# Optimization experiments

Hardware: AMD Instinct MI355X
Metric: run time of the kernel (lower is better)

The kernel has to match this reference:

```python
import jax, jax.numpy as jnp
import numpy as np

TOP_K = 2

def _moe_forward(x, gate_w, w1, w2, w3):
    # x: [B,S,H] -> tokens [T,H]
    B, S, H = x.shape
    xt = x.reshape(-1, H)                              # [T,H]
    T = xt.shape[0]
    E = gate_w.shape[0]
    # router
    logits = xt @ gate_w.T                             # [T,E]
    probs = jax.nn.softmax(logits.astype(jnp.float32), axis=-1)
    rw, sel = jax.lax.top_k(probs, TOP_K)              # [T,K]
    rw = rw / jnp.sum(rw, axis=-1, keepdims=True)
    # per-token per-expert combine weight (0 if expert not selected)
    combine = jnp.zeros((T, E), dtype=xt.dtype).at[
        jnp.arange(T)[:, None], sel].add(rw.astype(xt.dtype))  # [T,E]
    # dense per-expert SwiGLU FFN over all tokens (prefill path of module)
    h1 = jnp.einsum('th,efh->tef', xt, w1)             # [T,E,F]
    h3 = jnp.einsum('th,efh->tef', xt, w3)             # [T,E,F]
    g = jax.nn.silu(h1) * h3                           # [T,E,F]
    g = g * combine[:, :, None]                        # apply routing weight before down-proj
    out = jnp.einsum('tef,ehf->th', g, w2)             # [T,H]
    return out.reshape(B, S, H)


def setup_inputs() -> dict:
    key = jax.random.key(0)
    ks = jax.random.split(key, 5)
    B, S, H, F, E = 2, 2048, 1024, 3584, 8
    scale = 1.0 / np.sqrt(H)
    return {
        'hidden_states': jax.random.normal(ks[0], (B, S, H), jnp.float32),
        'gate_w': jax.random.normal(ks[1], (E, H), jnp.float32) * scale,
        'w1': jax.random.normal(ks[2], (E, F, H), jnp.float32) * scale,
        'w2': jax.random.normal(ks[3], (E, H, F), jnp.float32) * (1.0 / np.sqrt(F)),
        'w3': jax.random.normal(ks[4], (E, F, H), jnp.float32) * scale,
    }


def reference(hidden_states, gate_w, w1, w2, w3):
    return _moe_forward(hidden_states, gate_w, w1, w2, w3)
```

## Files before the change

### kernel.cpp

```cpp
#include <hip/hip_runtime.h>
#include <hip/hip_bf16.h>

#define TT   4096
#define HH   1024
#define FF   3584
#define EE   8
#define N13  7168
#define TKP  8192

typedef unsigned short u16;
typedef __attribute__((ext_vector_type(8))) short short8;
typedef __attribute__((ext_vector_type(4))) float floatx4;

__device__ __forceinline__ u16 f2b(float f) {
  union { float f; unsigned u; } v; v.f = f;
  unsigned r = v.u + 0x7FFFu + ((v.u >> 16) & 1u);
  return (u16)(r >> 16);
}

__device__ __forceinline__ void gld_lds16(const u16* g, u16* l) {
  __builtin_amdgcn_global_load_lds((const __attribute__((address_space(1))) unsigned int*)g,
                                   (__attribute__((address_space(3))) unsigned int*)l,
                                   16, 0, 0);
}

#define WAIT_LGKM0() asm volatile("s_waitcnt lgkmcnt(0)" ::: "memory")
#define WAIT_VM(n)   asm volatile("s_waitcnt vmcnt(" #n ")" ::: "memory")
#define BARRIER()    do { asm volatile("" ::: "memory"); __builtin_amdgcn_s_barrier(); asm volatile("" ::: "memory"); } while (0)

__global__ __launch_bounds__(256) void cvt_w13(const float* __restrict__ w1, const float* __restrict__ w3,
                                               ushort4* __restrict__ w13i) {
  int i = blockIdx.x * 256 + threadIdx.x;
  const int perE = N13 * (HH / 4);
  int e = i / perE;
  int rem = i - e * perE;
  int n = rem / (HH / 4);
  int h4 = rem - n * (HH / 4);
  int f = ((n >> 5) << 4) + (n & 15);
  int sel = (n >> 4) & 1;
  const float* base = sel ? w3 : w1;
  const float4* src = ((const float4*)(base + (size_t)(e * FF + f) * HH)) + h4;
  float4 v = *src;
  ushort4 o; o.x = f2b(v.x); o.y = f2b(v.y); o.z = f2b(v.z); o.w = f2b(v.w);
  w13i[i] = o;
}

__global__ __launch_bounds__(256) void cvt_w2(const float4* __restrict__ in, ushort4* __restrict__ outp) {
  int i = blockIdx.x * 256 + threadIdx.x;
  float4 v = in[i];
  ushort4 o; o.x = f2b(v.x); o.y = f2b(v.y); o.z = f2b(v.z); o.w = f2b(v.w);
  outp[i] = o;
}

__global__ __launch_bounds__(256) void router(const float* __restrict__ x, const float* __restrict__ gw,
                                              int* __restrict__ cnt, int* __restrict__ tok_list,
                                              float* __restrict__ wt_list, u16* __restrict__ xb) {
  int lane = threadIdx.x & 63;
  int wv = threadIdx.x >> 6;
  int t = blockIdx.x * 4 + wv;
  const float* xp = x + (size_t)t * HH;
  u16* xbp = xb + (size_t)t * HH;
  float acc[EE];
#pragma unroll
  for (int e = 0; e < EE; e++) acc[e] = 0.f;
  for (int h = lane; h < HH; h += 64) {
    float xv = xp[h];
    xbp[h] = f2b(xv);
#pragma unroll
    for (int e = 0; e < EE; e++) acc[e] += xv * gw[e * HH + h];
  }
#pragma unroll
  for (int e = 0; e < EE; e++) {
#pragma unroll
    for (int off = 32; off > 0; off >>= 1) acc[e] += __shfl_xor(acc[e], off, 64);
  }
  if (lane == 0) {
    int i1 = 0;
#pragma unroll
    for (int e = 1; e < EE; e++) if (acc[e] > acc[i1]) i1 = e;
    int i2 = -1;
#pragma unroll
    for (int e = 0; e < EE; e++) {
      if (e == i1) continue;
      if (i2 < 0 || acc[e] > acc[i2]) i2 = e;
    }
    float wA = 1.f / (1.f + __expf(acc[i2] - acc[i1]));
    float wB = 1.f - wA;
    int p1 = atomicAdd(cnt + i1, 1);
    tok_list[i1 * TT + p1] = t; wt_list[i1 * TT + p1] = wA;
    int p2 = atomicAdd(cnt + i2, 1);
    tok_list[i2 * TT + p2] = t; wt_list[i2 * TT + p2] = wB;
  }
}

__global__ void mk_offsets(const int* __restrict__ cnt, int* __restrict__ offs) {
  if (threadIdx.x == 0) {
    int s = 0;
    for (int e = 0; e < EE; e++) { offs[e] = s; s += cnt[e]; }
  }
}

__global__ __launch_bounds__(256) void pairmap(const int* __restrict__ cnt, const int* __restrict__ offs,
                                               const int* __restrict__ tok_list,
                                               int* __restrict__ tokp) {
  int i = blockIdx.x * 256 + threadIdx.x;
  int e = i >> 12;
  int s = i & (TT - 1);
  if (s < cnt[e]) {
    tokp[offs[e] + s] = tok_list[i];
  }
}

__global__ __launch_bounds__(512, 2) void gemm_a(const u16* __restrict__ xb, const u16* __restrict__ w13i,
                                                 const int* __restrict__ cnt, const int* __restrict__ offs,
                                                 const int* __restrict__ tok_list, const float* __restrict__ wt_list,
                                                 u16* __restrict__ gbuf) {
  const int fid = blockIdx.y * 28 + blockIdx.x;
  const int swz = (fid & 7) * 448 + (fid >> 3);
  const int ntile = swz % 28;
  const int yy = swz / 28;
  const int e = yy >> 4;
  const int rt = yy & 15;
  const int cn = cnt[e];
  if (rt * 256 >= cn) return;

  extern __shared__ char dynsmem[];
  u16* As = (u16*)dynsmem;
  u16* Bs = (u16*)(dynsmem + 65536);
  int* toks = (int*)(dynsmem + 131072);
  float* wts = (float*)(dynsmem + 131072 + 1024);

  const int tid = threadIdx.x;
  if (tid < 256) {
    int r = rt * 256 + tid;
    if (r >= cn) r = cn - 1;
    toks[tid] = tok_list[e * TT + r];
    wts[tid] = wt_list[e * TT + r];
  }
  __syncthreads();

  const int l = (tid & 7) ^ ((tid >> 3) & 7);
  const int dst0 = tid * 8;
  const u16* aS[4];
  const u16* bS[4];
#pragma unroll
  for (int i = 0; i < 4; i++) {
    int row = (tid >> 3) + i * 64;
    aS[i] = xb + (size_t)toks[row] * HH + l * 8;
    bS[i] = w13i + ((size_t)e * N13 + (size_t)ntile * 256 + row) * HH + l * 8;
  }

  auto STAGE = [&](int kt) {
    int b = (kt & 1) * 16384;
#pragma unroll
    for (int i = 0; i < 4; i++) {
      gld_lds16(aS[i] + kt * 64, As + b + dst0 + i * 4096);
      gld_lds16(bS[i] + kt * 64, Bs + b + dst0 + i * 4096);
    }
  };

  const int lane = tid & 63;
  const int wv = tid >> 6;
  const int wr = (wv >> 2) * 128;
  const int wc = (wv & 3) * 64;
  const int fr = lane & 15;
  const int fk8 = lane >> 4;

  floatx4 acc[8][4];
#pragma unroll
  for (int mi = 0; mi < 8; mi++)
#pragma unroll
    for (int ni = 0; ni < 4; ni++)
#pragma unroll
      for (int q = 0; q < 4; q++) acc[mi][ni][q] = 0.f;

  STAGE(0);
  STAGE(1);
  WAIT_VM(8);
  BARRIER();

  for (int t = 0; t < 16; t++) {
    const u16* Ab = As + (t & 1) * 16384;
    const u16* Bb = Bs + (t & 1) * 16384;
    __builtin_amdgcn_s_setprio(1);
#pragma unroll
    for (int ks = 0; ks < 2; ks++) {
      const int co = ((ks * 4 + fk8) ^ (fr & 7)) * 8;
      short8 af[8];
#pragma unroll
      for (int mi = 0; mi < 8; mi++)
        af[mi] = *(const short8*)&Ab[(wr + mi * 16 + fr) * 64 + co];
#pragma unroll
      for (int ni = 0; ni < 4; ni++) {
        short8 bf = *(const short8*)&Bb[(wc + ni * 16 + fr) * 64 + co];
#pragma unroll
        for (int mi = 0; mi < 8; mi++)
          acc[mi][ni] = __builtin_amdgcn_mfma_f32_16x16x32_bf16(af[mi], bf, acc[mi][ni], 0, 0, 0);
      }
    }
    __builtin_amdgcn_s_setprio(0);
    WAIT_LGKM0();
    BARRIER();
    if (t + 2 < 16) {
      STAGE(t + 2);
      WAIT_VM(8);
    } else {
      WAIT_VM(0);
    }
    BARRIER();
  }

  const int gofs = offs[e];
  const int cl = lane & 15;
  const int qr = (lane >> 4) * 4;
#pragma unroll
  for (int mi = 0; mi < 8; mi++) {
#pragma unroll
    for (int q = 0; q < 4; q++) {
      int r = wr + mi * 16 + qr + q;
      int gr = rt * 256 + r;
      if (gr < cn) {
        float w = wts[r];
        u16* dst = gbuf + (size_t)(gofs + gr) * FF + (size_t)ntile * 128 + (wc >> 1) + cl;
#pragma unroll
        for (int pg = 0; pg < 2; pg++) {
          float h1 = acc[mi][2 * pg][q];
          float h3 = acc[mi][2 * pg + 1][q];
          float s = h1 / (1.f + __expf(-h1));
          dst[pg * 16] = f2b(s * h3 * w);
        }
      }
    }
  }
}

__global__ __launch_bounds__(512, 2) void gemm_b(const u16* __restrict__ g, const u16* __restrict__ w2b,
                                                 const int* __restrict__ cnt, const int* __restrict__ offs,
                                                 const int* __restrict__ tokp, float* __restrict__ out) {
  const int fid = blockIdx.y * 8 + blockIdx.x;
  const int swz = (fid & 7) * 128 + (fid >> 3);
  const int ntile = swz % 8;
  const int yy = swz / 8;
  const int e = yy >> 4;
  const int rt = yy & 15;
  const int cn = cnt[e];
  if (rt * 256 >= cn) return;
  const int gofs = offs[e];

  extern __shared__ char dynsmem[];
  u16* As = (u16*)dynsmem;
  u16* Bs = (u16*)(dynsmem + 65536);
  int* toks = (int*)(dynsmem + 65536 + 32768);

  const int tid = threadIdx.x;
  if (tid < 256) {
    int r = rt * 256 + tid;
    if (r >= cn) r = cn - 1;
    toks[tid] = tokp[gofs + r];
  }
  __syncthreads();

  const int l = (tid & 7) ^ ((tid >> 3) & 7);
  const int dst0 = tid * 8;
  const u16* aS[4];
  const u16* bS[2];
#pragma unroll
  for (int i = 0; i < 4; i++) {
    int row = (tid >> 3) + i * 64;
    int gr = rt * 256 + row;
    if (gr >= cn) gr = cn - 1;
    aS[i] = g + (size_t)(gofs + gr) * FF + l * 8;
  }
#pragma unroll
  for (int i = 0; i < 2; i++) {
    int row = (tid >> 3) + i * 64;
    bS[i] = w2b + ((size_t)e * HH + (size_t)ntile * 128 + row) * FF + l * 8;
  }

  auto STAGE = [&](int kt) {
    int ba = (kt & 1) * 16384;
    int bb = (kt & 1) * 8192;
#pragma unroll
    for (int i = 0; i < 4; i++) gld_lds16(aS[i] + kt * 64, As + ba + dst0 + i * 4096);
#pragma unroll
    for (int i = 0; i < 2; i++) gld_lds16(bS[i] + kt * 64, Bs + bb + dst0 + i * 4096);
  };

  const int lane = tid & 63;
  const int wv = tid >> 6;
  const int wr = (wv >> 1) * 64;
  const int wc = (wv & 1) * 64;
  const int fr = lane & 15;
  const int fk8 = lane >> 4;

  floatx4 acc[4][4];
#pragma unroll
  for (int mi = 0; mi < 4; mi++)
#pragma unroll
    for (int ni = 0; ni < 4; ni++)
#pragma unroll
      for (int q = 0; q < 4; q++) acc[mi][ni][q] = 0.f;

  STAGE(0);
  STAGE(1);
  WAIT_VM(6);
  BARRIER();

  for (int t = 0; t < 56; t++) {
    const u16* Ab = As + (t & 1) * 16384;
    const u16* Bb = Bs + (t & 1) * 8192;
    __builtin_amdgcn_s_setprio(1);
#pragma unroll
    for (int ks = 0; ks < 2; ks++) {
      const int co = ((ks * 4 + fk8) ^ (fr & 7)) * 8;
      short8 af[4];
#pragma unroll
      for (int mi = 0; mi < 4; mi++)
        af[mi] = *(const short8*)&Ab[(wr + mi * 16 + fr) * 64 + co];
#pragma unroll
      for (int ni = 0; ni < 4; ni++) {
        short8 bf = *(const short8*)&Bb[(wc + ni * 16 + fr) * 64 + co];
#pragma unroll
        for (int mi = 0; mi < 4; mi++)
          acc[mi][ni] = __builtin_amdgcn_mfma_f32_16x16x32_bf16(af[mi], bf, acc[mi][ni], 0, 0, 0);
      }
    }
    __builtin_amdgcn_s_setprio(0);
    WAIT_LGKM0();
    BARRIER();
    if (t + 2 < 56) {
      STAGE(t + 2);
      WAIT_VM(6);
    } else {
      WAIT_VM(0);
    }
    BARRIER();
  }

  const int cl = lane & 15;
  const int qr = (lane >> 4) * 4;
#pragma unroll
  for (int mi = 0; mi < 4; mi++) {
#pragma unroll
    for (int q = 0; q < 4; q++) {
      int r = wr + mi * 16 + qr + q;
      int gr = rt * 256 + r;
      if (gr < cn) {
        int tk = toks[r];
        float* dst = out + (size_t)tk * HH + (size_t)ntile * 128 + wc + cl;
#pragma unroll
        for (int ni = 0; ni < 4; ni++) atomicAdd(dst + ni * 16, acc[mi][ni][q]);
      }
    }
  }
}

extern "C" void kernel_launch(void* const* d_in, const int* in_sizes, int n_in,
                              void* d_out, int out_size, void* d_ws, size_t ws_size,
                              hipStream_t stream) {
  const float* x  = (const float*)d_in[0];
  const float* gw = (const float*)d_in[1];
  const float* w1 = (const float*)d_in[2];
  const float* w2 = (const float*)d_in[3];
  const float* w3 = (const float*)d_in[4];
  float* out = (float*)d_out;

  char* ws = (char*)d_ws;
  u16* xb    = (u16*)ws;  ws += (size_t)TT * HH * 2;
  u16* w13i  = (u16*)ws;  ws += (size_t)EE * N13 * HH * 2;
  u16* w2b   = (u16*)ws;  ws += (size_t)EE * HH * FF * 2;
  u16* gbuf  = (u16*)ws;  ws += (size_t)TKP * FF * 2;
  int* cnt   = (int*)ws;  ws += 256;
  int* offs  = (int*)ws;  ws += 256;
  int* tok_list = (int*)ws;   ws += (size_t)EE * TT * 4;
  float* wt_list = (float*)ws; ws += (size_t)EE * TT * 4;
  int* tokp  = (int*)ws;  ws += (size_t)TKP * 4;

  const int A_SMEM = 65536 + 65536 + 1024 + 1024;
  const int B_SMEM = 65536 + 32768 + 1024;
  hipFuncSetAttribute((const void*)gemm_a, hipFuncAttributeMaxDynamicSharedMemorySize, A_SMEM);
  hipFuncSetAttribute((const void*)gemm_b, hipFuncAttributeMaxDynamicSharedMemorySize, B_SMEM);

  hipMemsetAsync(cnt, 0, 256, stream);
  hipMemsetAsync(out, 0, (size_t)TT * HH * 4, stream);

  cvt_w13<<<(EE * N13 * (HH / 4)) / 256, 256, 0, stream>>>(w1, w3, (ushort4*)w13i);
  cvt_w2<<<(EE * HH * (FF / 4)) / 256, 256, 0, stream>>>((const float4*)w2, (ushort4*)w2b);

  router<<<TT / 4, 256, 0, stream>>>(x, gw, cnt, tok_list, wt_list, xb);
  mk_offsets<<<1, 64, 0, stream>>>(cnt, offs);
  pairmap<<<(EE * TT) / 256, 256, 0, stream>>>(cnt, offs, tok_list, tokp);

  gemm_a<<<dim3(28, 128), 512, A_SMEM, stream>>>(xb, w13i, cnt, offs, tok_list, wt_list, gbuf);
  gemm_b<<<dim3(8, 128), 512, B_SMEM, stream>>>(gbuf, w2b, cnt, offs, tokp, out);
}
```

Measured before the change: 759.1 us.

## Split gemm_a main loop into four MFMA quadrants with interleaved LDS reads and prefetch

```diff
diff --git a/kernel.cpp b/kernel.cpp
--- a/kernel.cpp
+++ b/kernel.cpp
@@ -111,6 +111,30 @@
   }
 }
 
+#define READ_AF(AFR, QM)                                                          \
+  _Pragma("unroll")                                                               \
+  for (int mi = 0; mi < 4; mi++) {                                                \
+    AFR[mi][0] = *(const short8*)&Ab[(wr + ((QM)*4 + mi) * 16 + fr) * 64 + co0];  \
+    AFR[mi][1] = *(const short8*)&Ab[(wr + ((QM)*4 + mi) * 16 + fr) * 64 + co1];  \
+  }
+
+#define READ_BF(BFR, QN)                                                          \
+  _Pragma("unroll")                                                               \
+  for (int ni = 0; ni < 2; ni++) {                                                \
+    BFR[ni][0] = *(const short8*)&Bb[(wc + ((QN)*2 + ni) * 16 + fr) * 64 + co0];  \
+    BFR[ni][1] = *(const short8*)&Bb[(wc + ((QN)*2 + ni) * 16 + fr) * 64 + co1];  \
+  }
+
+#define MFMA_QUAD(AFR, BFR, QM, QN)                                               \
+  _Pragma("unroll")                                                               \
+  for (int ks = 0; ks < 2; ks++)                                                  \
+    _Pragma("unroll")                                                             \
+    for (int mi = 0; mi < 4; mi++)                                                \
+      _Pragma("unroll")                                                           \
+      for (int ni = 0; ni < 2; ni++)                                              \
+        acc[(QM)*4 + mi][(QN)*2 + ni] = __builtin_amdgcn_mfma_f32_16x16x32_bf16(  \
+            AFR[mi][ks], BFR[ni][ks], acc[(QM)*4 + mi][(QN)*2 + ni], 0, 0, 0);
+
 __global__ __launch_bounds__(512, 2) void gemm_a(const u16* __restrict__ xb, const u16* __restrict__ w13i,
                                                  const int* __restrict__ cnt, const int* __restrict__ offs,
                                                  const int* __restrict__ tok_list, const float* __restrict__ wt_list,
@@ -150,13 +174,15 @@
     bS[i] = w13i + ((size_t)e * N13 + (size_t)ntile * 256 + row) * HH + l * 8;
   }
 
-  auto STAGE = [&](int kt) {
+  auto STAGE_A = [&](int kt) {
     int b = (kt & 1) * 16384;
 #pragma unroll
-    for (int i = 0; i < 4; i++) {
-      gld_lds16(aS[i] + kt * 64, As + b + dst0 + i * 4096);
-      gld_lds16(bS[i] + kt * 64, Bs + b + dst0 + i * 4096);
-    }
+    for (int i = 0; i < 4; i++) gld_lds16(aS[i] + kt * 64, As + b + dst0 + i * 4096);
+  };
+  auto STAGE_B = [&](int kt) {
+    int b = (kt & 1) * 16384;
+#pragma unroll
+    for (int i = 0; i < 4; i++) gld_lds16(bS[i] + kt * 64, Bs + b + dst0 + i * 4096);
   };
 
   const int lane = tid & 63;
@@ -165,6 +191,8 @@
   const int wc = (wv & 3) * 64;
   const int fr = lane & 15;
   const int fk8 = lane >> 4;
+  const int co0 = ((0 + fk8) ^ (fr & 7)) * 8;
+  const int co1 = ((4 + fk8) ^ (fr & 7)) * 8;
 
   floatx4 acc[8][4];
 #pragma unroll
@@ -174,39 +202,45 @@
 #pragma unroll
       for (int q = 0; q < 4; q++) acc[mi][ni][q] = 0.f;
 
-  STAGE(0);
-  STAGE(1);
+  STAGE_B(0); STAGE_A(0);
+  STAGE_B(1); STAGE_A(1);
   WAIT_VM(8);
   BARRIER();
 
-  for (int t = 0; t < 16; t++) {
-    const u16* Ab = As + (t & 1) * 16384;
-    const u16* Bb = Bs + (t & 1) * 16384;
+  short8 af[4][2], bf0[2][2], bf1[2][2];
+  for (int g = 0; g < 16; g++) {
+    const u16* Ab = As + (g & 1) * 16384;
+    const u16* Bb = Bs + (g & 1) * 16384;
+    const bool pf = (g + 2 < 16);
+
+    READ_AF(af, 0)
+    READ_BF(bf0, 0)
+    WAIT_LGKM0(); __builtin_amdgcn_sched_barrier(0);
     __builtin_amdgcn_s_setprio(1);
-#pragma unroll
-    for (int ks = 0; ks < 2; ks++) {
-      const int co = ((ks * 4 + fk8) ^ (fr & 7)) * 8;
-      short8 af[8];
-#pragma unroll
-      for (int mi = 0; mi < 8; mi++)
-        af[mi] = *(const short8*)&Ab[(wr + mi * 16 + fr) * 64 + co];
-#pragma unroll
-      for (int ni = 0; ni < 4; ni++) {
-        short8 bf = *(const short8*)&Bb[(wc + ni * 16 + fr) * 64 + co];
-#pragma unroll
-        for (int mi = 0; mi < 8; mi++)
-          acc[mi][ni] = __builtin_amdgcn_mfma_f32_16x16x32_bf16(af[mi], bf, acc[mi][ni], 0, 0, 0);
-      }
-    }
+    MFMA_QUAD(af, bf0, 0, 0)
     __builtin_amdgcn_s_setprio(0);
-    WAIT_LGKM0();
-    BARRIER();
-    if (t + 2 < 16) {
-      STAGE(t + 2);
-      WAIT_VM(8);
-    } else {
-      WAIT_VM(0);
-    }
+    BARRIER();
+
+    READ_BF(bf1, 1)
+    WAIT_LGKM0(); __builtin_amdgcn_sched_barrier(0);
+    __builtin_amdgcn_s_setprio(1);
+    MFMA_QUAD(af, bf1, 0, 1)
+    __builtin_amdgcn_s_setprio(0);
+    BARRIER();
+
+    READ_AF(af, 1)
+    if (pf) STAGE_B(g + 2);
+    WAIT_LGKM0(); __builtin_amdgcn_sched_barrier(0);
+    __builtin_amdgcn_s_setprio(1);
+    MFMA_QUAD(af, bf1, 1, 1)
+    __builtin_amdgcn_s_setprio(0);
+    BARRIER();
+
+    if (pf) STAGE_A(g + 2);
+    __builtin_amdgcn_s_setprio(1);
+    MFMA_QUAD(af, bf0, 1, 0)
+    __builtin_amdgcn_s_setprio(0);
+    if (pf) { WAIT_VM(8); } else { WAIT_VM(0); }
     BARRIER();
   }
 
```

New measurement: 750.6 us. No clear change (-1.1%).
